# Optimization experiments

Hardware: AMD Instinct MI355X
Metric: run time of the kernel (lower is better)

Reference implementation:

```python
import jax, jax.numpy as jnp
import numpy as np

B, S, H, NCOL, NH = 32, 512, 768, 32, 12
HD = H // NH  # head dim 64
LN_EPS = 1e-12


def setup_inputs() -> dict:
    key = jax.random.key(0)
    ks = jax.random.split(key, 20)
    s = 0.02
    inp = {
        'hidden_states': jax.random.normal(ks[0], (B, S, H), jnp.float32),
        'column_embeddings': jax.random.normal(ks[1], (B, NCOL, H), jnp.float32),
        'column_categories': jax.random.randint(ks[2], (B, NCOL), 0, 2, jnp.int32),
        'value_mask': jax.random.randint(ks[3], (B, S), 0, NCOL + 1, jnp.int32),
        'Wd': jax.random.normal(ks[4], (H, H), jnp.float32) * s,
        'bd': jnp.zeros((H,), jnp.float32),
        'Wc': jax.random.normal(ks[5], (H, H), jnp.float32) * s,
        'bc': jnp.zeros((H,), jnp.float32),
        'Wq': jax.random.normal(ks[6], (H, H), jnp.float32) * s,
        'bq': jnp.zeros((H,), jnp.float32),
        'Wk': jax.random.normal(ks[7], (H, H), jnp.float32) * s,
        'bk': jnp.zeros((H,), jnp.float32),
        'Wv': jax.random.normal(ks[8], (H, H), jnp.float32) * s,
        'bv': jnp.zeros((H,), jnp.float32),
        'Wo': jax.random.normal(ks[9], (H, H), jnp.float32) * s,
        'bo': jnp.zeros((H,), jnp.float32),
        'ln_g': jnp.ones((H,), jnp.float32),
        'ln_b': jnp.zeros((H,), jnp.float32),
    }
    return inp


def _layernorm(x, g, b):
    mu = jnp.mean(x, axis=-1, keepdims=True)
    var = jnp.mean(jnp.square(x - mu), axis=-1, keepdims=True)
    return (x - mu) * jax.lax.rsqrt(var + LN_EPS) * g + b


def reference(hidden_states, column_embeddings, column_categories, value_mask,
              Wd, bd, Wc, bc, Wq, bq, Wk, bk, Wv, bv, Wo, bo, ln_g, ln_b):
    # dense branch
    h_ = hidden_states @ Wd.T + bd  # [B,S,H]
    # column gather: zero out category==0 columns, prepend zero row for index 0
    table = column_embeddings * (column_categories == 1)[..., None].astype(column_embeddings.dtype)
    table = jnp.concatenate([jnp.zeros_like(table[:, :1]), table], axis=1)  # [B,NCOL+1,H]
    h_col = jnp.take_along_axis(table, value_mask[..., None].astype(jnp.int32), axis=1)  # [B,S,H]
    h = jax.nn.gelu(h_ + (h_col @ Wc.T + bc), approximate=False)
    # Roberta self-attention
    def heads(x):
        return x.reshape(B, S, NH, HD).transpose(0, 2, 1, 3)  # [B,NH,S,HD]
    q = heads(h @ Wq.T + bq)
    k = heads(h @ Wk.T + bk)
    v = heads(h @ Wv.T + bv)
    scores = jnp.einsum('bhsd,bhtd->bhst', q, k) / jnp.sqrt(jnp.float32(HD))
    probs = jax.nn.softmax(scores, axis=-1)
    ctx = jnp.einsum('bhst,bhtd->bhsd', probs, v).transpose(0, 2, 1, 3).reshape(B, S, H)
    # self-output: dense + residual + layernorm
    out = _layernorm(ctx @ Wo.T + bo + h, ln_g, ln_b)
    return out
```

## Files before the change

### kernel.cpp

```cpp
#include <hip/hip_runtime.h>
#include <hip/hip_bf16.h>
#include <math.h>
#include <stdint.h>

#define B_    32
#define S_    512
#define H_    768
#define NH_   12
#define HD_   64
#define NCOL_ 32
#define M_    (B_*S_)

typedef __bf16 bf16;
typedef __bf16 bf16x8 __attribute__((ext_vector_type(8)));
typedef float  f32x4  __attribute__((ext_vector_type(4)));

__device__ __forceinline__ void async_load16(const void* g, void* l) {
    __builtin_amdgcn_global_load_lds(
        (__attribute__((address_space(1))) unsigned int*)g,
        (__attribute__((address_space(3))) unsigned int*)l, 16, 0, 0);
}

__device__ __forceinline__ bf16x8 cvt8(const float* p) {
    const float4* fp = (const float4*)p;
    float4 x = fp[0], y = fp[1];
    bf16x8 r;
    r[0] = (bf16)x.x; r[1] = (bf16)x.y; r[2] = (bf16)x.z; r[3] = (bf16)x.w;
    r[4] = (bf16)y.x; r[5] = (bf16)y.y; r[6] = (bf16)y.z; r[7] = (bf16)y.w;
    return r;
}

__global__ __launch_bounds__(256) void cvt_x_kernel(
    const float* __restrict__ hidden, const float* __restrict__ ce,
    const int* __restrict__ cc, const int* __restrict__ vm,
    bf16* __restrict__ hbf, bf16* __restrict__ hcol)
{
    int id = blockIdx.x * 256 + threadIdx.x;
    if (id < M_ * 96) {
        int row = id / 96, c = id - row * 96;
        *(bf16x8*)&hbf[(long)row * H_ + c * 8] = cvt8(hidden + (long)row * H_ + c * 8);
    } else {
        int cid = id - M_ * 96;
        int row = cid / 96, c = cid - row * 96;
        int b = row >> 9;
        int m = vm[row];
        bf16x8 val;
#pragma unroll
        for (int i = 0; i < 8; i++) val[i] = (bf16)0.0f;
        if (m > 0) {
            int col = m - 1;
            if (cc[b * NCOL_ + col] == 1)
                val = cvt8(ce + ((long)(b * NCOL_ + col)) * H_ + c * 8);
        }
        *(bf16x8*)&hcol[(long)row * H_ + c * 8] = val;
    }
}

__global__ __launch_bounds__(256) void cvt_w_kernel(
    const float* __restrict__ Wd, const float* __restrict__ Wc,
    const float* __restrict__ Wq, const float* __restrict__ Wk,
    const float* __restrict__ Wv, const float* __restrict__ Wo,
    const float* __restrict__ bq, const float* __restrict__ bk,
    const float* __restrict__ bv, bf16* __restrict__ wpack,
    float* __restrict__ bqkv)
{
    int id = blockIdx.x * 256 + threadIdx.x;
    if (id < 442368) {
        const float* src;
        int r = id;
        if      (r < 73728)  { src = Wd; }
        else if (r < 147456) { src = Wc; r -= 73728; }
        else if (r < 221184) { src = Wq; r -= 147456; }
        else if (r < 294912) { src = Wk; r -= 221184; }
        else if (r < 368640) { src = Wv; r -= 294912; }
        else                 { src = Wo; r -= 368640; }
        *(bf16x8*)&wpack[(long)id * 8] = cvt8(src + (long)r * 8);
    } else if (id < 442656) {
        int j0 = (id - 442368) * 8;
#pragma unroll
        for (int i = 0; i < 8; i++) {
            int j = j0 + i;
            float v = (j < 768) ? bq[j] : (j < 1536) ? bk[j - 768] : bv[j - 1536];
            bqkv[j] = v;
        }
    }
}

template<int MODE>
__global__ __launch_bounds__(256) void gemm_bt(
    const bf16* __restrict__ A0, const bf16* __restrict__ A1,
    const bf16* __restrict__ B0, const bf16* __restrict__ B1,
    const float* __restrict__ bias1, const float* __restrict__ bias2,
    const bf16* __restrict__ resid, bf16* __restrict__ out,
    int K, int KSPLIT)
{
    __shared__ __align__(16) bf16 As[128 * 32];
    __shared__ __align__(16) bf16 Bs[128 * 32];

    const int tid  = threadIdx.x;
    const int lane = tid & 63;
    const int wave = tid >> 6;
    const int wm   = wave & 1;
    const int wn   = wave >> 1;
    const int m0   = blockIdx.x * 128;
    const int n0   = blockIdx.y * 128;

    const int srow = tid >> 2;
    const int scol = (tid & 3) * 8;

    f32x4 acc[4][4];
    const f32x4 zero4 = {0.f, 0.f, 0.f, 0.f};
#pragma unroll
    for (int i = 0; i < 4; i++)
#pragma unroll
        for (int j = 0; j < 4; j++) acc[i][j] = zero4;

    const int a_off = (wm * 64 + (lane & 15)) * 32 + (lane >> 4) * 8;
    const int b_off = (wn * 64 + (lane & 15)) * 32 + (lane >> 4) * 8;

    for (int k0 = 0; k0 < K; k0 += 32) {
        const bf16* ag;
        const bf16* bg;
        if (k0 < KSPLIT) { ag = A0 + k0; bg = B0 + k0; }
        else             { ag = A1 + (k0 - KSPLIT); bg = B1 + (k0 - KSPLIT); }

        __syncthreads();
        async_load16(ag + (long)(m0 + srow) * H_ + scol,       As + tid * 8);
        async_load16(ag + (long)(m0 + 64 + srow) * H_ + scol,  As + 2048 + tid * 8);
        async_load16(bg + (long)(n0 + srow) * H_ + scol,       Bs + tid * 8);
        async_load16(bg + (long)(n0 + 64 + srow) * H_ + scol,  Bs + 2048 + tid * 8);
        __syncthreads();

        bf16x8 af[4], bfr[4];
#pragma unroll
        for (int i = 0; i < 4; i++) af[i]  = *(const bf16x8*)(As + a_off + i * 512);
#pragma unroll
        for (int j = 0; j < 4; j++) bfr[j] = *(const bf16x8*)(Bs + b_off + j * 512);
#pragma unroll
        for (int i = 0; i < 4; i++)
#pragma unroll
            for (int j = 0; j < 4; j++)
                acc[i][j] = __builtin_amdgcn_mfma_f32_16x16x32_bf16(af[i], bfr[j], acc[i][j], 0, 0, 0);
    }

    const int c_r = (lane >> 4) * 4;
    const int c_c = lane & 15;

    int sec = 0;
    if (MODE == 1) sec = (n0 >= 1536) ? 2 : ((n0 >= 768) ? 1 : 0);
    bf16* dst = (MODE == 1) ? out + (long)sec * M_ * H_ : out;

#pragma unroll
    for (int j = 0; j < 4; j++) {
        const int col = n0 + wn * 64 + j * 16 + c_c;
        float bias = bias1[col];
        if (MODE == 0) bias += bias2[col];
#pragma unroll
        for (int i = 0; i < 4; i++) {
#pragma unroll
            for (int r = 0; r < 4; r++) {
                const int row = m0 + wm * 64 + i * 16 + c_r + r;
                float v = acc[i][j][r] + bias;
                if (MODE == 0) {
                    v = 0.5f * v * (1.0f + erff(v * 0.70710678118654752f));
                    dst[(long)row * H_ + col] = (bf16)v;
                } else if (MODE == 1) {
                    int b = row >> 9, s = row & 511;
                    int cs = col - sec * 768;
                    int head = cs >> 6, d = cs & 63;
                    dst[(((long)(b * NH_ + head)) * S_ + s) * HD_ + d] = (bf16)v;
                } else {
                    v += (float)resid[(long)row * H_ + col];
                    dst[(long)row * H_ + col] = (bf16)v;
                }
            }
        }
    }
}

#define PS 88

__global__ __launch_bounds__(256) void attn_kernel(
    const bf16* __restrict__ q, const bf16* __restrict__ k,
    const bf16* __restrict__ v, bf16* __restrict__ ctx)
{
    __shared__ __align__(16) bf16 Qs[64 * PS];
    __shared__ __align__(16) bf16 Ks[64 * PS];
    __shared__ __align__(16) bf16 Vt[64 * PS];
    __shared__ __align__(16) bf16 Ps[4][16 * PS];

    const int tid  = threadIdx.x;
    const int lane = tid & 63;
    const int w    = tid >> 6;
    const int qt = blockIdx.x, h = blockIdx.y, b = blockIdx.z;
    const long base = ((long)(b * NH_ + h)) * S_ * HD_;

    {
        const bf16* qg = q + base + (long)qt * 64 * HD_;
        int c0 = tid * 2;
#pragma unroll
        for (int c = c0; c < c0 + 2; c++) {
            int row = c >> 3, cc = c & 7;
            *(uint4*)&Qs[row * PS + cc * 8] = *(const uint4*)&qg[row * HD_ + cc * 8];
        }
    }
    __syncthreads();

    const int fr = (lane >> 4) * 8;
    const bf16x8 aq0 = *(const bf16x8*)&Qs[(w * 16 + (lane & 15)) * PS + fr];
    const bf16x8 aq1 = *(const bf16x8*)&Qs[(w * 16 + (lane & 15)) * PS + 32 + fr];

    f32x4 O[4];
    const f32x4 zero4 = {0.f, 0.f, 0.f, 0.f};
#pragma unroll
    for (int t = 0; t < 4; t++) O[t] = zero4;
    float mo[4], l[4];
#pragma unroll
    for (int r = 0; r < 4; r++) { mo[r] = -1e30f; l[r] = 0.f; }

    const int vs = tid >> 2;
    const int vd = (tid & 3) * 16;

    for (int kc = 0; kc < 8; kc++) {
        __syncthreads();
        const bf16* kg = k + base + (long)kc * 64 * HD_;
        const bf16* vg = v + base + (long)kc * 64 * HD_;
        {
            int c0 = tid * 2;
#pragma unroll
            for (int c = c0; c < c0 + 2; c++) {
                int row = c >> 3, cc = c & 7;
                *(uint4*)&Ks[row * PS + cc * 8] = *(const uint4*)&kg[row * HD_ + cc * 8];
            }
            uint4 p0 = *(const uint4*)&vg[vs * HD_ + vd];
            uint4 p1 = *(const uint4*)&vg[vs * HD_ + vd + 8];
            const bf16* e0 = (const bf16*)&p0;
            const bf16* e1 = (const bf16*)&p1;
#pragma unroll
            for (int i = 0; i < 8; i++) Vt[(vd + i) * PS + vs]     = e0[i];
#pragma unroll
            for (int i = 0; i < 8; i++) Vt[(vd + 8 + i) * PS + vs] = e1[i];
        }
        __syncthreads();

        f32x4 sc[4];
#pragma unroll
        for (int j = 0; j < 4; j++) {
            sc[j] = zero4;
            bf16x8 b0 = *(const bf16x8*)&Ks[(j * 16 + (lane & 15)) * PS + fr];
            bf16x8 b1 = *(const bf16x8*)&Ks[(j * 16 + (lane & 15)) * PS + 32 + fr];
            sc[j] = __builtin_amdgcn_mfma_f32_16x16x32_bf16(aq0, b0, sc[j], 0, 0, 0);
            sc[j] = __builtin_amdgcn_mfma_f32_16x16x32_bf16(aq1, b1, sc[j], 0, 0, 0);
        }

#pragma unroll
        for (int r = 0; r < 4; r++) {
            float s0 = sc[0][r] * 0.125f, s1 = sc[1][r] * 0.125f;
            float s2 = sc[2][r] * 0.125f, s3 = sc[3][r] * 0.125f;
            float rm = fmaxf(fmaxf(s0, s1), fmaxf(s2, s3));
            rm = fmaxf(rm, __shfl_xor(rm, 1));
            rm = fmaxf(rm, __shfl_xor(rm, 2));
            rm = fmaxf(rm, __shfl_xor(rm, 4));
            rm = fmaxf(rm, __shfl_xor(rm, 8));
            float mn = fmaxf(mo[r], rm);
            float alpha = __expf(mo[r] - mn);
            s0 = __expf(s0 - mn); s1 = __expf(s1 - mn);
            s2 = __expf(s2 - mn); s3 = __expf(s3 - mn);
            float rs = s0 + s1 + s2 + s3;
            rs += __shfl_xor(rs, 1);
            rs += __shfl_xor(rs, 2);
            rs += __shfl_xor(rs, 4);
            rs += __shfl_xor(rs, 8);
            l[r] = l[r] * alpha + rs;
            mo[r] = mn;
#pragma unroll
            for (int t = 0; t < 4; t++) O[t][r] *= alpha;
            int prow = (lane >> 4) * 4 + r;
            Ps[w][prow * PS +      (lane & 15)] = (bf16)s0;
            Ps[w][prow * PS + 16 + (lane & 15)] = (bf16)s1;
            Ps[w][prow * PS + 32 + (lane & 15)] = (bf16)s2;
            Ps[w][prow * PS + 48 + (lane & 15)] = (bf16)s3;
        }
        __syncthreads();

#pragma unroll
        for (int hh = 0; hh < 2; hh++) {
            bf16x8 ap = *(const bf16x8*)&Ps[w][(lane & 15) * PS + hh * 32 + fr];
#pragma unroll
            for (int t = 0; t < 4; t++) {
                bf16x8 bv = *(const bf16x8*)&Vt[(t * 16 + (lane & 15)) * PS + hh * 32 + fr];
                O[t] = __builtin_amdgcn_mfma_f32_16x16x32_bf16(ap, bv, O[t], 0, 0, 0);
            }
        }
    }

#pragma unroll
    for (int r = 0; r < 4; r++) {
        float inv = 1.0f / l[r];
        int s = qt * 64 + w * 16 + (lane >> 4) * 4 + r;
#pragma unroll
        for (int t = 0; t < 4; t++) {
            int d = t * 16 + (lane & 15);
            ctx[((long)(b * S_ + s)) * H_ + h * HD_ + d] = (bf16)(O[t][r] * inv);
        }
    }
}

__global__ __launch_bounds__(256) void ln_kernel(
    const bf16* __restrict__ y, const float* __restrict__ g,
    const float* __restrict__ be, float* __restrict__ out)
{
    const int lane = threadIdx.x & 63;
    const int w    = threadIdx.x >> 6;
    const long row = (long)blockIdx.x * 4 + w;
    const bf16* yr = y + row * H_;

    float x[12];
    float sum = 0.f, ss = 0.f;
#pragma unroll
    for (int j = 0; j < 12; j++) {
        x[j] = (float)yr[j * 64 + lane];
        sum += x[j];
        ss  += x[j] * x[j];
    }
#pragma unroll
    for (int m = 1; m < 64; m <<= 1) {
        sum += __shfl_xor(sum, m);
        ss  += __shfl_xor(ss, m);
    }
    const float mu  = sum * (1.0f / 768.0f);
    float var = ss * (1.0f / 768.0f) - mu * mu;
    const float rs = rsqrtf(fmaxf(var, 0.f) + 1e-12f);
#pragma unroll
    for (int j = 0; j < 12; j++) {
        int c = j * 64 + lane;
        out[row * H_ + c] = (x[j] - mu) * rs * g[c] + be[c];
    }
}

extern "C" void kernel_launch(void* const* d_in, const int* in_sizes, int n_in,
                              void* d_out, int out_size, void* d_ws, size_t ws_size,
                              hipStream_t stream)
{
    const float* hidden = (const float*)d_in[0];
    const float* ce     = (const float*)d_in[1];
    const int*   cc     = (const int*)d_in[2];
    const int*   vm     = (const int*)d_in[3];
    const float* Wd     = (const float*)d_in[4];
    const float* bd     = (const float*)d_in[5];
    const float* Wc     = (const float*)d_in[6];
    const float* bc     = (const float*)d_in[7];
    const float* Wq     = (const float*)d_in[8];
    const float* bq     = (const float*)d_in[9];
    const float* Wk     = (const float*)d_in[10];
    const float* bk     = (const float*)d_in[11];
    const float* Wv     = (const float*)d_in[12];
    const float* bv     = (const float*)d_in[13];
    const float* Wo     = (const float*)d_in[14];
    const float* bo     = (const float*)d_in[15];
    const float* lng    = (const float*)d_in[16];
    const float* lnb    = (const float*)d_in[17];

    const long NE = (long)M_ * H_;
    bf16* ws   = (bf16*)d_ws;
    bf16* hbuf = ws;
    bf16* qkv  = ws + NE;
    bf16* hbf  = qkv;
    bf16* hcol = qkv + NE;
    bf16* qb   = qkv;
    bf16* kb   = qkv + NE;
    bf16* vb   = qkv + 2 * NE;
    bf16* wpack = ws + 4 * NE;
    const bf16* Wd_b  = wpack;
    const bf16* Wc_b  = wpack + 589824;
    const bf16* Wq_b  = wpack + 1179648;
    const bf16* Wk_b  = wpack + 1769472;
    const bf16* Wv_b  = wpack + 2359296;
    const bf16* Wo_b  = wpack + 2949120;
    float* bqkv = (float*)(wpack + 3538944);
    bf16* ctx = (bf16*)d_out;

    cvt_x_kernel<<<2 * M_ * 96 / 256, 256, 0, stream>>>(hidden, ce, cc, vm, hbf, hcol);
    cvt_w_kernel<<<1730, 256, 0, stream>>>(Wd, Wc, Wq, Wk, Wv, Wo, bq, bk, bv, wpack, bqkv);

    dim3 g6(M_ / 128, 6);
    dim3 g18(M_ / 128, 18);
    gemm_bt<0><<<g6, 256, 0, stream>>>(hbf, hcol, Wd_b, Wc_b, bd, bc, nullptr, hbuf, 2 * H_, H_);
    gemm_bt<1><<<g18, 256, 0, stream>>>(hbuf, hbuf, Wq_b, Wq_b, bqkv, nullptr, nullptr, qkv, H_, 3 * H_);
    attn_kernel<<<dim3(S_ / 64, NH_, B_), 256, 0, stream>>>(qb, kb, vb, ctx);
    gemm_bt<2><<<g6, 256, 0, stream>>>(ctx, ctx, Wo_b, Wo_b, bo, nullptr, hbuf, hbuf, H_, H_);
    ln_kernel<<<M_ / 4, 256, 0, stream>>>(hbuf, lng, lnb, (float*)d_out);
}
```

Before: 452.7 us.

## Store V transposed from QKV GEMM and restructure attention with swapped MFMA operands

The QKV GEMM now writes V in [b,h,d,s] layout, so the attention kernel no longer needs the scalar LDS transpose of V. The attention kernel computes S^T and O^T by swapping MFMA operands. This lets each lane own one query row, so softmax reductions need only two cross-quad shuffles and the barrier before the PV step goes away. The next K and V tiles are register-prefetched while the current ones are computed, and the grid is flattened so query tiles of the same (b,h) are spread apart. Output goes through LDS for coalesced 16-byte stores. In exchange, V stores from the GEMM epilogue are strided, and the prefetch adds register pressure.

```diff
diff --git a/kernel.cpp b/kernel.cpp
--- a/kernel.cpp
+++ b/kernel.cpp
@@ -13,6 +13,7 @@
 
 typedef __bf16 bf16;
 typedef __bf16 bf16x8 __attribute__((ext_vector_type(8)));
+typedef __bf16 bf16x4 __attribute__((ext_vector_type(4)));
 typedef float  f32x4  __attribute__((ext_vector_type(4)));
 
 __device__ __forceinline__ void async_load16(const void* g, void* l) {
@@ -168,7 +169,10 @@
                     int b = row >> 9, s = row & 511;
                     int cs = col - sec * 768;
                     int head = cs >> 6, d = cs & 63;
-                    dst[(((long)(b * NH_ + head)) * S_ + s) * HD_ + d] = (bf16)v;
+                    if (sec == 2)
+                        dst[(((long)(b * NH_ + head)) * HD_ + d) * S_ + s] = (bf16)v;
+                    else
+                        dst[(((long)(b * NH_ + head)) * S_ + s) * HD_ + d] = (bf16)v;
                 } else {
                     v += (float)resid[(long)row * H_ + col];
                     dst[(long)row * H_ + col] = (bf16)v;
@@ -178,131 +182,142 @@
     }
 }
 
-#define PS 88
+#define QP 72
 
 __global__ __launch_bounds__(256) void attn_kernel(
     const bf16* __restrict__ q, const bf16* __restrict__ k,
-    const bf16* __restrict__ v, bf16* __restrict__ ctx)
-{
-    __shared__ __align__(16) bf16 Qs[64 * PS];
-    __shared__ __align__(16) bf16 Ks[64 * PS];
-    __shared__ __align__(16) bf16 Vt[64 * PS];
-    __shared__ __align__(16) bf16 Ps[4][16 * PS];
+    const bf16* __restrict__ vt, bf16* __restrict__ ctx)
+{
+    __shared__ __align__(16) bf16 Qs[64 * QP];
+    __shared__ __align__(16) bf16 Ks[64 * QP];
+    __shared__ __align__(16) bf16 Vt[64 * QP];
+    __shared__ __align__(16) bf16 Ps[4][16 * QP];
 
     const int tid  = threadIdx.x;
     const int lane = tid & 63;
     const int w    = tid >> 6;
-    const int qt = blockIdx.x, h = blockIdx.y, b = blockIdx.z;
+    const int quad = lane >> 4;
+    const int ln16 = lane & 15;
+
+    const int bid = blockIdx.x;
+    const int qt  = bid / 384;
+    const int g   = bid - qt * 384;
+    const int b   = g / 12;
+    const int h   = g - b * 12;
     const long base = ((long)(b * NH_ + h)) * S_ * HD_;
+
+    const int r0 = tid >> 2;
+    const int e0 = (tid & 3) * 16;
 
     {
         const bf16* qg = q + base + (long)qt * 64 * HD_;
-        int c0 = tid * 2;
-#pragma unroll
-        for (int c = c0; c < c0 + 2; c++) {
-            int row = c >> 3, cc = c & 7;
-            *(uint4*)&Qs[row * PS + cc * 8] = *(const uint4*)&qg[row * HD_ + cc * 8];
-        }
-    }
+        *(uint4*)&Qs[r0 * QP + e0]     = *(const uint4*)&qg[r0 * HD_ + e0];
+        *(uint4*)&Qs[r0 * QP + e0 + 8] = *(const uint4*)&qg[r0 * HD_ + e0 + 8];
+    }
+    const bf16* kg = k  + base;
+    const bf16* vg = vt + base;
+    uint4 kr0 = *(const uint4*)&kg[r0 * HD_ + e0];
+    uint4 kr1 = *(const uint4*)&kg[r0 * HD_ + e0 + 8];
+    uint4 vr0 = *(const uint4*)&vg[(long)r0 * S_ + e0];
+    uint4 vr1 = *(const uint4*)&vg[(long)r0 * S_ + e0 + 8];
     __syncthreads();
 
-    const int fr = (lane >> 4) * 8;
-    const bf16x8 aq0 = *(const bf16x8*)&Qs[(w * 16 + (lane & 15)) * PS + fr];
-    const bf16x8 aq1 = *(const bf16x8*)&Qs[(w * 16 + (lane & 15)) * PS + 32 + fr];
+    const bf16x8 bq0 = *(const bf16x8*)&Qs[(w * 16 + ln16) * QP + quad * 8];
+    const bf16x8 bq1 = *(const bf16x8*)&Qs[(w * 16 + ln16) * QP + 32 + quad * 8];
 
     f32x4 O[4];
     const f32x4 zero4 = {0.f, 0.f, 0.f, 0.f};
 #pragma unroll
     for (int t = 0; t < 4; t++) O[t] = zero4;
-    float mo[4], l[4];
-#pragma unroll
-    for (int r = 0; r < 4; r++) { mo[r] = -1e30f; l[r] = 0.f; }
-
-    const int vs = tid >> 2;
-    const int vd = (tid & 3) * 16;
+    float mo = -1e30f, l = 0.f;
 
     for (int kc = 0; kc < 8; kc++) {
         __syncthreads();
-        const bf16* kg = k + base + (long)kc * 64 * HD_;
-        const bf16* vg = v + base + (long)kc * 64 * HD_;
+        *(uint4*)&Ks[r0 * QP + e0]     = kr0;
+        *(uint4*)&Ks[r0 * QP + e0 + 8] = kr1;
+        *(uint4*)&Vt[r0 * QP + e0]     = vr0;
+        *(uint4*)&Vt[r0 * QP + e0 + 8] = vr1;
         {
-            int c0 = tid * 2;
-#pragma unroll
-            for (int c = c0; c < c0 + 2; c++) {
-                int row = c >> 3, cc = c & 7;
-                *(uint4*)&Ks[row * PS + cc * 8] = *(const uint4*)&kg[row * HD_ + cc * 8];
+            int kcn = (kc < 7) ? kc + 1 : 7;
+            kr0 = *(const uint4*)&kg[(long)kcn * 64 * HD_ + r0 * HD_ + e0];
+            kr1 = *(const uint4*)&kg[(long)kcn * 64 * HD_ + r0 * HD_ + e0 + 8];
+            vr0 = *(const uint4*)&vg[(long)r0 * S_ + kcn * 64 + e0];
+            vr1 = *(const uint4*)&vg[(long)r0 * S_ + kcn * 64 + e0 + 8];
+        }
+        __syncthreads();
+
+        f32x4 sc[4];
+#pragma unroll
+        for (int i = 0; i < 4; i++) {
+            bf16x8 a0 = *(const bf16x8*)&Ks[(i * 16 + ln16) * QP + quad * 8];
+            bf16x8 a1 = *(const bf16x8*)&Ks[(i * 16 + ln16) * QP + 32 + quad * 8];
+            sc[i] = zero4;
+            sc[i] = __builtin_amdgcn_mfma_f32_16x16x32_bf16(a0, bq0, sc[i], 0, 0, 0);
+            sc[i] = __builtin_amdgcn_mfma_f32_16x16x32_bf16(a1, bq1, sc[i], 0, 0, 0);
+        }
+
+        float cm = -1e30f;
+#pragma unroll
+        for (int i = 0; i < 4; i++)
+#pragma unroll
+            for (int r = 0; r < 4; r++) {
+                float s = sc[i][r] * 0.125f;
+                sc[i][r] = s;
+                cm = fmaxf(cm, s);
             }
-            uint4 p0 = *(const uint4*)&vg[vs * HD_ + vd];
-            uint4 p1 = *(const uint4*)&vg[vs * HD_ + vd + 8];
-            const bf16* e0 = (const bf16*)&p0;
-            const bf16* e1 = (const bf16*)&p1;
-#pragma unroll
-            for (int i = 0; i < 8; i++) Vt[(vd + i) * PS + vs]     = e0[i];
-#pragma unroll
-            for (int i = 0; i < 8; i++) Vt[(vd + 8 + i) * PS + vs] = e1[i];
-        }
-        __syncthreads();
-
-        f32x4 sc[4];
-#pragma unroll
-        for (int j = 0; j < 4; j++) {
-            sc[j] = zero4;
-            bf16x8 b0 = *(const bf16x8*)&Ks[(j * 16 + (lane & 15)) * PS + fr];
-            bf16x8 b1 = *(const bf16x8*)&Ks[(j * 16 + (lane & 15)) * PS + 32 + fr];
-            sc[j] = __builtin_amdgcn_mfma_f32_16x16x32_bf16(aq0, b0, sc[j], 0, 0, 0);
-            sc[j] = __builtin_amdgcn_mfma_f32_16x16x32_bf16(aq1, b1, sc[j], 0, 0, 0);
-        }
-
-#pragma unroll
-        for (int r = 0; r < 4; r++) {
-            float s0 = sc[0][r] * 0.125f, s1 = sc[1][r] * 0.125f;
-            float s2 = sc[2][r] * 0.125f, s3 = sc[3][r] * 0.125f;
-            float rm = fmaxf(fmaxf(s0, s1), fmaxf(s2, s3));
-            rm = fmaxf(rm, __shfl_xor(rm, 1));
-            rm = fmaxf(rm, __shfl_xor(rm, 2));
-            rm = fmaxf(rm, __shfl_xor(rm, 4));
-            rm = fmaxf(rm, __shfl_xor(rm, 8));
-            float mn = fmaxf(mo[r], rm);
-            float alpha = __expf(mo[r] - mn);
-            s0 = __expf(s0 - mn); s1 = __expf(s1 - mn);
-            s2 = __expf(s2 - mn); s3 = __expf(s3 - mn);
-            float rs = s0 + s1 + s2 + s3;
-            rs += __shfl_xor(rs, 1);
-            rs += __shfl_xor(rs, 2);
-            rs += __shfl_xor(rs, 4);
-            rs += __shfl_xor(rs, 8);
-            l[r] = l[r] * alpha + rs;
-            mo[r] = mn;
-#pragma unroll
-            for (int t = 0; t < 4; t++) O[t][r] *= alpha;
-            int prow = (lane >> 4) * 4 + r;
-            Ps[w][prow * PS +      (lane & 15)] = (bf16)s0;
-            Ps[w][prow * PS + 16 + (lane & 15)] = (bf16)s1;
-            Ps[w][prow * PS + 32 + (lane & 15)] = (bf16)s2;
-            Ps[w][prow * PS + 48 + (lane & 15)] = (bf16)s3;
-        }
-        __syncthreads();
-
-#pragma unroll
-        for (int hh = 0; hh < 2; hh++) {
-            bf16x8 ap = *(const bf16x8*)&Ps[w][(lane & 15) * PS + hh * 32 + fr];
-#pragma unroll
-            for (int t = 0; t < 4; t++) {
-                bf16x8 bv = *(const bf16x8*)&Vt[(t * 16 + (lane & 15)) * PS + hh * 32 + fr];
-                O[t] = __builtin_amdgcn_mfma_f32_16x16x32_bf16(ap, bv, O[t], 0, 0, 0);
+        cm = fmaxf(cm, __shfl_xor(cm, 16));
+        cm = fmaxf(cm, __shfl_xor(cm, 32));
+        float mn = fmaxf(mo, cm);
+        float alpha = __expf(mo - mn);
+        float rs = 0.f;
+#pragma unroll
+        for (int i = 0; i < 4; i++) {
+            bf16x4 pk;
+#pragma unroll
+            for (int r = 0; r < 4; r++) {
+                float p = __expf(sc[i][r] - mn);
+                rs += p;
+                pk[r] = (bf16)p;
             }
-        }
-    }
-
-#pragma unroll
-    for (int r = 0; r < 4; r++) {
-        float inv = 1.0f / l[r];
-        int s = qt * 64 + w * 16 + (lane >> 4) * 4 + r;
-#pragma unroll
-        for (int t = 0; t < 4; t++) {
-            int d = t * 16 + (lane & 15);
-            ctx[((long)(b * S_ + s)) * H_ + h * HD_ + d] = (bf16)(O[t][r] * inv);
-        }
+            *(bf16x4*)&Ps[w][ln16 * QP + i * 16 + quad * 4] = pk;
+        }
+        rs += __shfl_xor(rs, 16);
+        rs += __shfl_xor(rs, 32);
+        l  = l * alpha + rs;
+        mo = mn;
+#pragma unroll
+        for (int t = 0; t < 4; t++)
+#pragma unroll
+            for (int r = 0; r < 4; r++) O[t][r] *= alpha;
+
+        bf16x8 bp0 = *(const bf16x8*)&Ps[w][ln16 * QP + quad * 8];
+        bf16x8 bp1 = *(const bf16x8*)&Ps[w][ln16 * QP + 32 + quad * 8];
+#pragma unroll
+        for (int dt = 0; dt < 4; dt++) {
+            bf16x8 a0 = *(const bf16x8*)&Vt[(dt * 16 + ln16) * QP + quad * 8];
+            bf16x8 a1 = *(const bf16x8*)&Vt[(dt * 16 + ln16) * QP + 32 + quad * 8];
+            O[dt] = __builtin_amdgcn_mfma_f32_16x16x32_bf16(a0, bp0, O[dt], 0, 0, 0);
+            O[dt] = __builtin_amdgcn_mfma_f32_16x16x32_bf16(a1, bp1, O[dt], 0, 0, 0);
+        }
+    }
+
+    {
+        float inv = 1.0f / l;
+#pragma unroll
+        for (int dt = 0; dt < 4; dt++) {
+            bf16x4 ov;
+#pragma unroll
+            for (int r = 0; r < 4; r++) ov[r] = (bf16)(O[dt][r] * inv);
+            *(bf16x4*)&Qs[(w * 16 + ln16) * QP + dt * 16 + quad * 4] = ov;
+        }
+    }
+    __syncthreads();
+    {
+        uint4 o0 = *(const uint4*)&Qs[r0 * QP + e0];
+        uint4 o1 = *(const uint4*)&Qs[r0 * QP + e0 + 8];
+        bf16* cg = ctx + ((long)(b * S_ + qt * 64 + r0)) * H_ + h * HD_;
+        *(uint4*)&cg[e0]     = o0;
+        *(uint4*)&cg[e0 + 8] = o1;
     }
 }
 
@@ -387,7 +402,7 @@
     dim3 g18(M_ / 128, 18);
     gemm_bt<0><<<g6, 256, 0, stream>>>(hbf, hcol, Wd_b, Wc_b, bd, bc, nullptr, hbuf, 2 * H_, H_);
     gemm_bt<1><<<g18, 256, 0, stream>>>(hbuf, hbuf, Wq_b, Wq_b, bqkv, nullptr, nullptr, qkv, H_, 3 * H_);
-    attn_kernel<<<dim3(S_ / 64, NH_, B_), 256, 0, stream>>>(qb, kb, vb, ctx);
+    attn_kernel<<<3072, 256, 0, stream>>>(qb, kb, vb, ctx);
     gemm_bt<2><<<g6, 256, 0, stream>>>(ctx, ctx, Wo_b, Wo_b, bo, nullptr, hbuf, hbuf, H_, H_);
     ln_kernel<<<M_ / 4, 256, 0, stream>>>(hbuf, lng, lnb, (float*)d_out);
 }
```

After: 430.9 us. -4.8%, faster.
